# Optimization experiments

Hardware: AMD Instinct MI355X
Metric: run time of the kernel (lower is better)

The kernel has to match this reference:

```python
import jax, jax.numpy as jnp
import numpy as np

B, C, H, W = 8, 512, 32, 32
NUM_HEADS = 8
HEAD_DIM = C // NUM_HEADS


def setup_inputs() -> dict:
    key = jax.random.key(0)
    k1, k2, k3 = jax.random.split(key, 3)
    query = jax.random.normal(k1, (B, C, H, W), dtype=jnp.float32)
    key_value = jax.random.normal(k2, (B, C, H, W), dtype=jnp.float32)
    # Linear(dim, 3*dim): store as [C, 3C] so y = x @ W + b
    W_qkv = jax.random.normal(k3, (C, 3 * C), dtype=jnp.float32) * (C ** -0.5)
    b_qkv = jnp.zeros((3 * C,), dtype=jnp.float32)
    return {"query": query, "key_value": key_value, "W_qkv": W_qkv, "b_qkv": b_qkv}


def reference(query, key_value, W_qkv, b_qkv):
    Bb, Cc, Hh, Ww = query.shape
    seq = Hh * Ww
    scale = HEAD_DIM ** -0.5

    # [B, C, H, W] -> [B, S, C]
    q_seq = query.reshape(Bb, Cc, seq).transpose(0, 2, 1)
    kv_seq = key_value.reshape(Bb, Cc, seq).transpose(0, 2, 1)

    # Original calls full qkv_proj and slices; math == projecting with sliced weights.
    q = q_seq @ W_qkv[:, :Cc] + b_qkv[:Cc]
    k = kv_seq @ W_qkv[:, Cc:2 * Cc] + b_qkv[Cc:2 * Cc]
    v = kv_seq @ W_qkv[:, 2 * Cc:] + b_qkv[2 * Cc:]

    def heads(x):  # [B, S, C] -> [B, nH, S, hd]
        return x.reshape(Bb, seq, NUM_HEADS, HEAD_DIM).transpose(0, 2, 1, 3)

    q, k, v = heads(q), heads(k), heads(v)
    attn = jnp.einsum('bhqd,bhkd->bhqk', q, k) * scale
    attn = jax.nn.softmax(attn, axis=-1)  # dropout: identity in eval
    out = jnp.einsum('bhqk,bhkd->bhqd', attn, v)
    # [B, nH, S, hd] -> [B, S, C] -> [B, C, H, W]
    out = out.transpose(0, 2, 1, 3).reshape(Bb, seq, Cc)
    return out.transpose(0, 2, 1).reshape(Bb, Cc, Hh, Ww)
```

## Files before the change

### kernel.cpp

```cpp
#include <hip/hip_runtime.h>
#include <hip/hip_bf16.h>

using short4v = __attribute__((ext_vector_type(4))) short;
using short8  = __attribute__((ext_vector_type(8))) short;
using uint2v  = __attribute__((ext_vector_type(2))) unsigned int;
using f32x4   = __attribute__((ext_vector_type(4))) float;

static constexpr int CDIM = 512;
static constexpr float KSCALE = 0.125f * 1.44269504088896341f;

__device__ __forceinline__ short f2bf(float f) {
  unsigned u = __builtin_bit_cast(unsigned, f);
  u = (u + 0x7fffu + ((u >> 16) & 1u)) >> 16;
  return (short)(unsigned short)u;
}
__device__ __forceinline__ unsigned pack_bf16(float a, float b) {
  return (unsigned)(unsigned short)f2bf(a) | ((unsigned)(unsigned short)f2bf(b) << 16);
}

#define GLOAD_LDS16(gp, lp)                                                              \
  __builtin_amdgcn_global_load_lds((const __attribute__((address_space(1))) void*)(gp),  \
                                   (__attribute__((address_space(3))) void*)(lp), 16, 0, 0)
#define MFMA16(a, b, c) __builtin_amdgcn_mfma_f32_16x16x32_bf16((a), (b), (c), 0, 0, 0)
#define WAIT_LGKM0() __builtin_amdgcn_s_waitcnt(0xc07f)

__global__ __launch_bounds__(256) void prep_transpose(const float* __restrict__ query,
                                                      const float* __restrict__ keyv,
                                                      const float* __restrict__ Wqkv,
                                                      short* __restrict__ Xq_t,
                                                      short* __restrict__ Xkv_t,
                                                      short* __restrict__ W_t) {
  __shared__ float tile[64 * 65];
  const int id = blockIdx.x;
  const float* s; short* d; int R, C, r0, c0;
  if (id < 2048) {
    const int which = id >> 10;
    int rem = id & 1023;
    const int b = rem >> 7; rem &= 127;
    R = 512; C = 1024;
    s = (which ? keyv : query) + (size_t)b * 512 * 1024;
    d = (which ? Xkv_t : Xq_t) + (size_t)b * 512 * 1024;
    r0 = (rem >> 4) * 64; c0 = (rem & 15) * 64;
  } else {
    const int rem = id - 2048;
    R = 512; C = 1536; s = Wqkv; d = W_t;
    r0 = (rem / 24) * 64; c0 = (rem % 24) * 64;
  }
  const int t  = threadIdx.x;
  const int rr = t >> 4;
  const int c4 = (t & 15) * 4;
#pragma unroll
  for (int i = 0; i < 4; ++i) {
    const int r = rr + i * 16;
    f32x4 v = *(const f32x4*)(s + (size_t)(r0 + r) * C + c0 + c4);
#pragma unroll
    for (int j = 0; j < 4; ++j) tile[(c4 + j) * 65 + r] = v[j];
  }
  __syncthreads();
  const int r8 = (t & 7) * 8;
#pragma unroll
  for (int i = 0; i < 2; ++i) {
    const int c = (t >> 3) + i * 32;
    short8 pk;
#pragma unroll
    for (int j = 0; j < 8; ++j) pk[j] = f2bf(tile[c * 65 + r8 + j]);
    *(short8*)(d + (size_t)(c0 + c) * R + r0 + r8) = pk;
  }
}

__global__ __launch_bounds__(256, 2) void qkv_gemm(const short* __restrict__ Xq,
                                                   const short* __restrict__ Xkv,
                                                   const short* __restrict__ Wt,
                                                   const float* __restrict__ bias,
                                                   short* __restrict__ Qg,
                                                   short* __restrict__ Kg,
                                                   short* __restrict__ Vt) {
  __shared__ short Asm[128 * 64];
  __shared__ short Bsm[256 * 64];
  __shared__ short epi[4 * 1152];
  const int n0 = blockIdx.x * 256;
  const int m0 = blockIdx.y * 128;
  const short* A = (n0 < CDIM) ? Xq : Xkv;
  const int t = threadIdx.x;
  const int w = t >> 6, l = t & 63;
  const int wm = w & 1, wn = w >> 1;
  const int lc = l & 15, lr = l >> 4;

  f32x4 acc[4][8];
#pragma unroll
  for (int i = 0; i < 4; ++i)
#pragma unroll
    for (int j = 0; j < 8; ++j) acc[i][j] = (f32x4){0.f, 0.f, 0.f, 0.f};

  for (int kb = 0; kb < 8; ++kb) {
    const int k0 = kb * 64;
#pragma unroll
    for (int i = 0; i < 4; ++i) {
      const int Qi = (w * 4 + i) * 64 + l;
      const int row = Qi >> 3, u = Qi & 7;
      GLOAD_LDS16(A + (size_t)(m0 + row) * CDIM + k0 + ((u ^ (row & 7)) * 8), &Asm[Qi * 8]);
    }
#pragma unroll
    for (int i = 0; i < 8; ++i) {
      const int Qi = (w * 8 + i) * 64 + l;
      const int row = Qi >> 3, u = Qi & 7;
      GLOAD_LDS16(Wt + (size_t)(n0 + row) * CDIM + k0 + ((u ^ (row & 7)) * 8), &Bsm[Qi * 8]);
    }
    __syncthreads();
#pragma unroll
    for (int kc = 0; kc < 2; ++kc) {
      short8 af[4], bfr[8];
#pragma unroll
      for (int mt = 0; mt < 4; ++mt) {
        const int row = wm * 64 + mt * 16 + lc;
        af[mt] = *(const short8*)(&Asm[(row * 8 + ((kc * 4 + lr) ^ (row & 7))) * 8]);
      }
#pragma unroll
      for (int nt = 0; nt < 8; ++nt) {
        const int row = wn * 128 + nt * 16 + lc;
        bfr[nt] = *(const short8*)(&Bsm[(row * 8 + ((kc * 4 + lr) ^ (row & 7))) * 8]);
      }
#pragma unroll
      for (int mt = 0; mt < 4; ++mt)
#pragma unroll
        for (int nt = 0; nt < 8; ++nt)
          acc[mt][nt] = MFMA16(af[mt], bfr[nt], acc[mt][nt]);
    }
    __syncthreads();
  }

  const int M0 = m0 + wm * 64;
  const int bb = M0 >> 10, s0 = M0 & 1023;
  const int N0 = n0 + wn * 128;
  float bv[8];
#pragma unroll
  for (int nt = 0; nt < 8; ++nt) bv[nt] = bias[N0 + nt * 16 + lc];
  short* slab = epi + w * 1152;

#pragma unroll
  for (int hi = 0; hi < 2; ++hi) {
    const int hg = (N0 >> 6) + hi;
    const int part = hg >> 3, hh = hg & 7;
    const int nb = hi * 4;
    if (part < 2) {
      const float osc = part ? 1.f : KSCALE;
      short* obase = (part ? Kg : Qg) + (size_t)(bb * 8 + hh) * 65536 + (size_t)s0 * 64;
#pragma unroll
      for (int mt = 0; mt < 4; ++mt) {
#pragma unroll
        for (int ntL = 0; ntL < 4; ++ntL)
#pragma unroll
          for (int r = 0; r < 4; ++r)
            slab[(lr * 4 + r) * 72 + ntL * 16 + lc] =
                f2bf((acc[mt][nb + ntL][r] + bv[nb + ntL]) * osc);
        WAIT_LGKM0();
#pragma unroll
        for (int i = 0; i < 2; ++i) {
          const int slot = i * 64 + l;
          const int m_l = slot >> 3, n8 = (slot & 7) * 8;
          short8 vv = *(const short8*)(&slab[m_l * 72 + n8]);
          *(short8*)(obase + (size_t)(mt * 16 + m_l) * 64 + n8) = vv;
        }
        WAIT_LGKM0();
      }
    } else {
      short* vbase = Vt + (size_t)(bb * 8 + hh) * 65536;
#pragma unroll
      for (int ntL = 0; ntL < 4; ++ntL) {
#pragma unroll
        for (int mt = 0; mt < 4; ++mt)
#pragma unroll
          for (int r = 0; r < 4; ++r)
            slab[lc * 72 + mt * 16 + lr * 4 + r] = f2bf(acc[mt][nb + ntL][r] + bv[nb + ntL]);
        WAIT_LGKM0();
#pragma unroll
        for (int i = 0; i < 2; ++i) {
          const int slot = i * 64 + l;
          const int dloc = slot >> 3, ch = (slot & 7) * 8;
          short8 vv = *(const short8*)(&slab[dloc * 72 + ch]);
          *(short8*)(vbase + (size_t)(ntL * 16 + dloc) * 1024 + s0 + ch) = vv;
        }
        WAIT_LGKM0();
      }
    }
  }
}

__global__ __launch_bounds__(256, 2) void flash_attn(const short* __restrict__ Qg,
                                                     const short* __restrict__ Kg,
                                                     const short* __restrict__ Vt,
                                                     float* __restrict__ out) {
  __shared__ alignas(16) short smem[17408];
  short* Ksm = smem;
  short* Vsm = smem + 4096;
  const int bh = blockIdx.x;
  const int b = bh >> 3, h = bh & 7;
  const int q0 = blockIdx.y * 128;
  const int t = threadIdx.x;
  const int w = t >> 6, l = t & 63;
  const int quad = l >> 4, l15 = l & 15;
  short* Pw = smem + 8192 + w * 2304;

  const short* Qbase = Qg + (size_t)bh * 65536;
  const short* Kbase = Kg + (size_t)bh * 65536;
  const short* Vbase = Vt + (size_t)bh * 65536;

  short8 bq[2][2];
#pragma unroll
  for (int qs = 0; qs < 2; ++qs) {
    const short* qrow = Qbase + (size_t)(q0 + qs * 64 + w * 16 + l15) * 64;
    bq[qs][0] = *(const short8*)(qrow + quad * 8);
    bq[qs][1] = *(const short8*)(qrow + 32 + quad * 8);
  }

  float lp[2] = {0.f, 0.f};
  f32x4 Oac[2][4];
#pragma unroll
  for (int qs = 0; qs < 2; ++qs)
#pragma unroll
    for (int dt = 0; dt < 4; ++dt) Oac[qs][dt] = (f32x4){0.f, 0.f, 0.f, 0.f};

  for (int it = 0; it < 16; ++it) {
    const int kk0 = it * 64;
#pragma unroll
    for (int i = 0; i < 2; ++i) {
      const int Qi = (w * 2 + i) * 64 + l;
      const int sr = Qi >> 3, u = Qi & 7;
      GLOAD_LDS16(Kbase + (size_t)(kk0 + sr) * 64 + (u ^ (sr & 7)) * 8, &Ksm[Qi * 8]);
      GLOAD_LDS16(Vbase + (size_t)sr * 1024 + kk0 + (u ^ (sr & 7)) * 8, &Vsm[Qi * 8]);
    }
    __syncthreads();

    short8 kf[2][4];
#pragma unroll
    for (int c = 0; c < 2; ++c)
#pragma unroll
      for (int nt = 0; nt < 4; ++nt) {
        const int srow = nt * 16 + l15;
        kf[c][nt] = *(const short8*)(&Ksm[(srow * 8 + ((c * 4 + quad) ^ (srow & 7))) * 8]);
      }

#pragma unroll
    for (int qs = 0; qs < 2; ++qs) {
      f32x4 st[4];
#pragma unroll
      for (int nt = 0; nt < 4; ++nt) {
        st[nt] = (f32x4){0.f, 0.f, 0.f, 0.f};
#pragma unroll
        for (int c = 0; c < 2; ++c) st[nt] = MFMA16(kf[c][nt], bq[qs][c], st[nt]);
      }
      short* Ps = Pw + qs * 1152;
#pragma unroll
      for (int nt = 0; nt < 4; ++nt) {
        float p0 = __builtin_amdgcn_exp2f(st[nt][0]);
        float p1 = __builtin_amdgcn_exp2f(st[nt][1]);
        float p2 = __builtin_amdgcn_exp2f(st[nt][2]);
        float p3 = __builtin_amdgcn_exp2f(st[nt][3]);
        lp[qs] += (p0 + p1) + (p2 + p3);
        uint2v pk;
        pk[0] = pack_bf16(p0, p1);
        pk[1] = pack_bf16(p2, p3);
        *(uint2v*)(&Ps[l15 * 72 + (nt * 4 + quad) * 4]) = pk;
      }
    }
    WAIT_LGKM0();

#pragma unroll
    for (int c = 0; c < 2; ++c) {
      short8 pb0 = *(const short8*)(&Pw[l15 * 72 + (c * 8 + quad * 2) * 4]);
      short8 pb1 = *(const short8*)(&Pw[1152 + l15 * 72 + (c * 8 + quad * 2) * 4]);
#pragma unroll
      for (int dt = 0; dt < 4; ++dt) {
        const int drow = dt * 16 + l15;
        short8 vf = *(const short8*)(&Vsm[(drow * 8 + ((c * 4 + quad) ^ (drow & 7))) * 8]);
        Oac[0][dt] = MFMA16(vf, pb0, Oac[0][dt]);
        Oac[1][dt] = MFMA16(vf, pb1, Oac[1][dt]);
      }
    }
    __syncthreads();
  }

#pragma unroll
  for (int qs = 0; qs < 2; ++qs) {
    float lv = lp[qs];
    lv += __shfl_xor(lv, 16, 64);
    lv += __shfl_xor(lv, 32, 64);
    const float rinv = 1.f / lv;
    float* ob = out + ((size_t)(b * 512 + h * 64)) * 1024 + q0 + qs * 64 + w * 16 + l15;
#pragma unroll
    for (int dt = 0; dt < 4; ++dt)
#pragma unroll
      for (int r = 0; r < 4; ++r)
        ob[(size_t)(dt * 16 + quad * 4 + r) * 1024] = Oac[qs][dt][r] * rinv;
  }
}

extern "C" void kernel_launch(void* const* d_in, const int* in_sizes, int n_in,
                              void* d_out, int out_size, void* d_ws, size_t ws_size,
                              hipStream_t stream) {
  const float* query = (const float*)d_in[0];
  const float* keyv  = (const float*)d_in[1];
  const float* Wqkv  = (const float*)d_in[2];
  const float* bqkv  = (const float*)d_in[3];
  float* out = (float*)d_out;
  short* ws  = (short*)d_ws;

  short* Xq_t  = ws;
  short* Xkv_t = ws + 4194304;
  short* W_t   = ws + 8388608;
  short* Qg    = ws + 9175040;
  short* Kg    = ws + 13369344;
  short* Vt    = ws + 17563648;

  prep_transpose<<<dim3(2240), 256, 0, stream>>>(query, keyv, Wqkv, Xq_t, Xkv_t, W_t);
  qkv_gemm<<<dim3(6, 64, 1), 256, 0, stream>>>(Xq_t, Xkv_t, W_t, bqkv, Qg, Kg, Vt);
  flash_attn<<<dim3(64, 8, 1), 256, 0, stream>>>(Qg, Kg, Vt, out);
}
```

Before: 134.0 us.

## Load two KV tiles per barrier in attention and remap GEMM block order

The flash-attention loop now stages two 64-key K/V tiles into doubled shared memory before each barrier. This halves the load-wait sync points and issues more outstanding global loads per wait, at the cost of more LDS per block, which may reduce occupancy. The QKV GEMM grid becomes 1D with a permuted tile mapping that spreads M blocks across XCDs and improves L2 reuse of weight tiles.

New measurement: 133.2 us. No clear change (-0.6%).

```diff
diff --git a/kernel.cpp b/kernel.cpp
--- a/kernel.cpp
+++ b/kernel.cpp
@@ -78,8 +78,11 @@
   __shared__ short Asm[128 * 64];
   __shared__ short Bsm[256 * 64];
   __shared__ short epi[4 * 1152];
-  const int n0 = blockIdx.x * 256;
-  const int m0 = blockIdx.y * 128;
+  const int id = blockIdx.x;
+  const int n_blk = id >> 6;
+  const int m_blk = ((id & 7) << 3) | ((id >> 3) & 7);
+  const int n0 = n_blk << 8;
+  const int m0 = m_blk << 7;
   const short* A = (n0 < CDIM) ? Xq : Xkv;
   const int t = threadIdx.x;
   const int w = t >> 6, l = t & 63;
@@ -190,16 +193,16 @@
                                                      const short* __restrict__ Kg,
                                                      const short* __restrict__ Vt,
                                                      float* __restrict__ out) {
-  __shared__ alignas(16) short smem[17408];
+  __shared__ alignas(16) short smem[25600];
   short* Ksm = smem;
-  short* Vsm = smem + 4096;
+  short* Vsm = smem + 8192;
   const int bh = blockIdx.x;
   const int b = bh >> 3, h = bh & 7;
   const int q0 = blockIdx.y * 128;
   const int t = threadIdx.x;
   const int w = t >> 6, l = t & 63;
   const int quad = l >> 4, l15 = l & 15;
-  short* Pw = smem + 8192 + w * 2304;
+  short* Pw = smem + 16384 + w * 2304;
 
   const short* Qbase = Qg + (size_t)bh * 65536;
   const short* Kbase = Kg + (size_t)bh * 65536;
@@ -220,64 +223,74 @@
 #pragma unroll
     for (int dt = 0; dt < 4; ++dt) Oac[qs][dt] = (f32x4){0.f, 0.f, 0.f, 0.f};
 
-  for (int it = 0; it < 16; ++it) {
-    const int kk0 = it * 64;
-#pragma unroll
-    for (int i = 0; i < 2; ++i) {
-      const int Qi = (w * 2 + i) * 64 + l;
-      const int sr = Qi >> 3, u = Qi & 7;
-      GLOAD_LDS16(Kbase + (size_t)(kk0 + sr) * 64 + (u ^ (sr & 7)) * 8, &Ksm[Qi * 8]);
-      GLOAD_LDS16(Vbase + (size_t)sr * 1024 + kk0 + (u ^ (sr & 7)) * 8, &Vsm[Qi * 8]);
+  for (int it2 = 0; it2 < 8; ++it2) {
+#pragma unroll
+    for (int half = 0; half < 2; ++half) {
+      const int kk0 = (it2 * 2 + half) * 64;
+      short* Kd = Ksm + half * 4096;
+      short* Vd = Vsm + half * 4096;
+#pragma unroll
+      for (int i = 0; i < 2; ++i) {
+        const int Qi = (w * 2 + i) * 64 + l;
+        const int sr = Qi >> 3, u = Qi & 7;
+        GLOAD_LDS16(Kbase + (size_t)(kk0 + sr) * 64 + (u ^ (sr & 7)) * 8, &Kd[Qi * 8]);
+        GLOAD_LDS16(Vbase + (size_t)sr * 1024 + kk0 + (u ^ (sr & 7)) * 8, &Vd[Qi * 8]);
+      }
     }
     __syncthreads();
 
-    short8 kf[2][4];
-#pragma unroll
-    for (int c = 0; c < 2; ++c)
-#pragma unroll
-      for (int nt = 0; nt < 4; ++nt) {
-        const int srow = nt * 16 + l15;
-        kf[c][nt] = *(const short8*)(&Ksm[(srow * 8 + ((c * 4 + quad) ^ (srow & 7))) * 8]);
-      }
-
-#pragma unroll
-    for (int qs = 0; qs < 2; ++qs) {
-      f32x4 st[4];
-#pragma unroll
-      for (int nt = 0; nt < 4; ++nt) {
-        st[nt] = (f32x4){0.f, 0.f, 0.f, 0.f};
-#pragma unroll
-        for (int c = 0; c < 2; ++c) st[nt] = MFMA16(kf[c][nt], bq[qs][c], st[nt]);
-      }
-      short* Ps = Pw + qs * 1152;
-#pragma unroll
-      for (int nt = 0; nt < 4; ++nt) {
-        float p0 = __builtin_amdgcn_exp2f(st[nt][0]);
-        float p1 = __builtin_amdgcn_exp2f(st[nt][1]);
-        float p2 = __builtin_amdgcn_exp2f(st[nt][2]);
-        float p3 = __builtin_amdgcn_exp2f(st[nt][3]);
-        lp[qs] += (p0 + p1) + (p2 + p3);
-        uint2v pk;
-        pk[0] = pack_bf16(p0, p1);
-        pk[1] = pack_bf16(p2, p3);
-        *(uint2v*)(&Ps[l15 * 72 + (nt * 4 + quad) * 4]) = pk;
-      }
-    }
-    WAIT_LGKM0();
-
-#pragma unroll
-    for (int c = 0; c < 2; ++c) {
-      short8 pb0 = *(const short8*)(&Pw[l15 * 72 + (c * 8 + quad * 2) * 4]);
-      short8 pb1 = *(const short8*)(&Pw[1152 + l15 * 72 + (c * 8 + quad * 2) * 4]);
-#pragma unroll
-      for (int dt = 0; dt < 4; ++dt) {
-        const int drow = dt * 16 + l15;
-        short8 vf = *(const short8*)(&Vsm[(drow * 8 + ((c * 4 + quad) ^ (drow & 7))) * 8]);
-        Oac[0][dt] = MFMA16(vf, pb0, Oac[0][dt]);
-        Oac[1][dt] = MFMA16(vf, pb1, Oac[1][dt]);
-      }
-    }
-    __syncthreads();
+#pragma unroll
+    for (int half = 0; half < 2; ++half) {
+      const short* Kh = Ksm + half * 4096;
+      const short* Vh = Vsm + half * 4096;
+      short8 kf[2][4];
+#pragma unroll
+      for (int c = 0; c < 2; ++c)
+#pragma unroll
+        for (int nt = 0; nt < 4; ++nt) {
+          const int srow = nt * 16 + l15;
+          kf[c][nt] = *(const short8*)(&Kh[(srow * 8 + ((c * 4 + quad) ^ (srow & 7))) * 8]);
+        }
+
+#pragma unroll
+      for (int qs = 0; qs < 2; ++qs) {
+        f32x4 st[4];
+#pragma unroll
+        for (int nt = 0; nt < 4; ++nt) {
+          st[nt] = (f32x4){0.f, 0.f, 0.f, 0.f};
+#pragma unroll
+          for (int c = 0; c < 2; ++c) st[nt] = MFMA16(kf[c][nt], bq[qs][c], st[nt]);
+        }
+        short* Ps = Pw + qs * 1152;
+#pragma unroll
+        for (int nt = 0; nt < 4; ++nt) {
+          float p0 = __builtin_amdgcn_exp2f(st[nt][0]);
+          float p1 = __builtin_amdgcn_exp2f(st[nt][1]);
+          float p2 = __builtin_amdgcn_exp2f(st[nt][2]);
+          float p3 = __builtin_amdgcn_exp2f(st[nt][3]);
+          lp[qs] += (p0 + p1) + (p2 + p3);
+          uint2v pk;
+          pk[0] = pack_bf16(p0, p1);
+          pk[1] = pack_bf16(p2, p3);
+          *(short4v*)(&Ps[l15 * 72 + (nt * 4 + quad) * 4]) = __builtin_bit_cast(short4v, pk);
+        }
+      }
+      WAIT_LGKM0();
+
+#pragma unroll
+      for (int c = 0; c < 2; ++c) {
+        short8 pb0 = *(const short8*)(&Pw[l15 * 72 + (c * 8 + quad * 2) * 4]);
+        short8 pb1 = *(const short8*)(&Pw[1152 + l15 * 72 + (c * 8 + quad * 2) * 4]);
+#pragma unroll
+        for (int dt = 0; dt < 4; ++dt) {
+          const int drow = dt * 16 + l15;
+          short8 vf = *(const short8*)(&Vh[(drow * 8 + ((c * 4 + quad) ^ (drow & 7))) * 8]);
+          Oac[0][dt] = MFMA16(vf, pb0, Oac[0][dt]);
+          Oac[1][dt] = MFMA16(vf, pb1, Oac[1][dt]);
+        }
+      }
+      __syncthreads();
+    }
   }
 
 #pragma unroll
@@ -313,6 +326,6 @@
   short* Vt    = ws + 17563648;
 
   prep_transpose<<<dim3(2240), 256, 0, stream>>>(query, keyv, Wqkv, Xq_t, Xkv_t, W_t);
-  qkv_gemm<<<dim3(6, 64, 1), 256, 0, stream>>>(Xq_t, Xkv_t, W_t, bqkv, Qg, Kg, Vt);
+  qkv_gemm<<<dim3(384), 256, 0, stream>>>(Xq_t, Xkv_t, W_t, bqkv, Qg, Kg, Vt);
   flash_attn<<<dim3(64, 8, 1), 256, 0, stream>>>(Qg, Kg, Vt, out);
 }
```
